# Kernel tuning notes

Measured on AMD Instinct MI355X. Metric: run time of the kernel, lower is better.

The kernel has to match this reference:

```python
import jax, jax.numpy as jnp
import numpy as np

PREFIX = 20000
LEAF = 50000
NONLEAF = 50000
NUMD = 8 * NONLEAF  # 400000 fine-depth nodes
C = 256


def setup_inputs() -> dict:
    key = jax.random.key(0)
    k1, k2 = jax.random.split(key)
    n_rows = PREFIX + LEAF + NUMD
    x = jax.random.normal(k1, (n_rows, C), dtype=jnp.float32)
    # xavier-uniform-like init for Downsample weights (C_out, C_in, 8)
    limit = float(np.sqrt(6.0 / (C + C * 8)))
    weights = jax.random.uniform(k2, (C, C, 8), dtype=jnp.float32,
                                 minval=-limit, maxval=limit)
    # children at depth-1: alternate leaf (-1) / non-leaf (+1) -> exactly LEAF leaves
    children = jnp.where(jnp.arange(LEAF + NONLEAF) % 2 == 0, -1, 1).astype(jnp.int32)
    return {"x": x, "weights": weights, "children": children,
            "numd": NUMD, "leaf_num": LEAF}


def reference(x, weights, children, numd, leaf_num):
    c = x.shape[1]
    # Downsample: groups of 8 fine nodes -> one coarse node.
    # torch: x.view(-1, 8*C) @ weights.flatten(1).t()
    outd = x[-numd:].reshape(-1, 8 * c) @ weights.reshape(c, 8 * c).T  # [numd/8, C]

    leaf_mask = children < 0                      # [nnum_prev]
    lm = leaf_mask.astype(jnp.int32)
    rank_leaf = jnp.cumsum(lm) - lm               # rank among leaf positions
    nlm = 1 - lm
    rank_nonleaf = jnp.cumsum(nlm) - nlm          # rank among non-leaf positions
    # out[leaf_mask] = x[-leaf_num-numd:-numd]; out[~leaf_mask] = outd
    idx = jnp.where(leaf_mask, rank_leaf, leaf_num + rank_nonleaf)
    x_leaf = x[-(leaf_num + numd):-numd]          # [leaf_num, C]
    combined = jnp.concatenate([x_leaf, outd], axis=0)
    merged = combined[idx]                        # [nnum_prev, C]

    prefix = x.shape[0] - leaf_num - numd
    return jnp.concatenate([x[:prefix], merged], axis=0)
```

## Files before the change

### kernel.cpp

```cpp
#include <hip/hip_runtime.h>
#include <hip/hip_bf16.h>

#define PREFIX_N 20000
#define LEAF_N   50000
#define CH_N     100000
#define CCOL     256
#define GK       2048
#define GM       50000
#define BM       64
#define BKF      128
#define NST      (GK / BKF)
#define TILES    ((GM + BM - 1) / BM)
#define NCOPYB   512
#define COPYROWS 70000

typedef float  f32x4v __attribute__((ext_vector_type(4)));
typedef __bf16 bf16x8 __attribute__((ext_vector_type(8)));
typedef short  s16x8  __attribute__((ext_vector_type(8)));

static __device__ __forceinline__ unsigned pk2(float a, float b) {
  __hip_bfloat16 ha = __float2bfloat16(a);
  __hip_bfloat16 hb = __float2bfloat16(b);
  unsigned short sa = __builtin_bit_cast(unsigned short, ha);
  unsigned short sb = __builtin_bit_cast(unsigned short, hb);
  return (unsigned)sa | ((unsigned)sb << 16);
}
static __device__ __forceinline__ uint4 pack8(const float4& x, const float4& y) {
  uint4 r;
  r.x = pk2(x.x, x.y); r.y = pk2(x.z, x.w);
  r.z = pk2(y.x, y.y); r.w = pk2(y.z, y.w);
  return r;
}

#define GLDS16(g, l) __builtin_amdgcn_global_load_lds(                      \
    (const __attribute__((address_space(1))) void*)(g),                     \
    (__attribute__((address_space(3))) void*)(l), 16, 0, 0)

__global__ __launch_bounds__(256) void prep_kernel(const float* __restrict__ W,
                                                   unsigned short* __restrict__ Wb,
                                                   const int* __restrict__ ch,
                                                   int* __restrict__ cnt) {
  if (blockIdx.x < 256) {
    int i = blockIdx.x * 256 + threadIdx.x;
    float4 a = ((const float4*)W)[i * 2];
    float4 b = ((const float4*)W)[i * 2 + 1];
    *(uint4*)&Wb[i * 8] = pack8(a, b);
  } else {
    int blk = blockIdx.x - 256;
    int gi = blk * 256 + threadIdx.x;
    int lm = (gi < CH_N && ch[gi] < 0) ? 1 : 0;
    unsigned long long mask = __ballot(lm);
    __shared__ int wsum[4];
    int lane = threadIdx.x & 63, w = threadIdx.x >> 6;
    if (lane == 0) wsum[w] = __popcll(mask);
    __syncthreads();
    if (threadIdx.x == 0) cnt[blk] = wsum[0] + wsum[1] + wsum[2] + wsum[3];
  }
}

__global__ __launch_bounds__(512) void scan_blocks(const int* __restrict__ cnt,
                                                   int* __restrict__ boff, int nb) {
  __shared__ int s[512];
  int t = threadIdx.x;
  int v = (t < nb) ? cnt[t] : 0;
  s[t] = v;
  __syncthreads();
  for (int d = 1; d < 512; d <<= 1) {
    int add = (t >= d) ? s[t - d] : 0;
    __syncthreads();
    s[t] += add;
    __syncthreads();
  }
  if (t < nb) boff[t] = s[t] - v;
}

__global__ __launch_bounds__(256) void rank_kernel(const int* __restrict__ ch,
                                                   const int* __restrict__ boff, int n,
                                                   int* __restrict__ rowof,
                                                   int* __restrict__ leafof) {
  int gi = blockIdx.x * 256 + threadIdx.x;
  int lane = threadIdx.x & 63, w = threadIdx.x >> 6;
  int lm = (gi < n && ch[gi] < 0) ? 1 : 0;
  unsigned long long mask = __ballot(lm);
  int lrank = __popcll(mask & ((1ull << lane) - 1ull));
  __shared__ int wcnt[4];
  if (lane == 63) wcnt[w] = lrank + lm;
  __syncthreads();
  int woff = 0;
  for (int i = 0; i < w; ++i) woff += wcnt[i];
  if (gi < n) {
    int rl = boff[blockIdx.x] + woff + lrank;
    if (lm) leafof[rl] = gi;
    else    rowof[gi - rl] = gi;
  }
}

__global__ __launch_bounds__(256, 2) void main_kernel(const float* __restrict__ x,
                                                      const float* __restrict__ A,
                                                      const unsigned short* __restrict__ Wb,
                                                      const int* __restrict__ rowof,
                                                      const int* __restrict__ leafof,
                                                      float* __restrict__ out) {
  __shared__ float Al[2][BM][BKF];
  __shared__ int tgt[BM];

  const int tid  = threadIdx.x;
  const int lane = tid & 63;
  const int w    = tid >> 6;

  if (blockIdx.x >= TILES) {
    int cb = blockIdx.x - TILES;
    for (int r0 = cb * 4; r0 < COPYROWS; r0 += NCOPYB * 4) {
      int j = r0 + w;
      if (j >= COPYROWS) break;
      const float* src;
      float* dst;
      if (j < PREFIX_N) {
        src = x + (size_t)j * CCOL;
        dst = out + (size_t)j * CCOL;
      } else {
        int r = j - PREFIX_N;
        src = x + (size_t)(PREFIX_N + r) * CCOL;
        dst = out + (size_t)(PREFIX_N + leafof[r]) * CCOL;
      }
      ((float4*)dst)[lane] = ((const float4*)src)[lane];
    }
    return;
  }

  const int tile = blockIdx.x;
  const int wn   = w;
  const int lr   = lane & 15, lq = lane >> 4;

  if (tid < BM) {
    int m = tile * BM + tid;
    tgt[tid] = (m < GM) ? (PREFIX_N + rowof[m]) : -1;
  }

  const float* asrc[8];
  int myrow = w * 16 + (lane >> 5);
#pragma unroll
  for (int i = 0; i < 8; ++i) {
    int r  = myrow + 2 * i;
    int gr = tile * BM + r;
    if (gr >= GM) gr = GM - 1;
    int chunk = (lane & 31) ^ (r & 7);
    asrc[i] = A + (size_t)gr * GK + chunk * 4;
  }

  const unsigned short* bb[4];
#pragma unroll
  for (int fn = 0; fn < 4; ++fn)
    bb[fn] = Wb + (size_t)(wn * 64 + fn * 16 + lr) * GK + lq * 8;

  f32x4v acc[4][4] = {};

#define ISSUE_A(kt_, buf_)                                                   \
  { _Pragma("unroll") for (int i = 0; i < 8; ++i)                            \
      GLDS16(asrc[i] + (kt_) * BKF, (char*)&Al[(buf_)][w * 16 + 2 * i][0]); }

  ISSUE_A(0, 0);
  ISSUE_A(1, 1);

#pragma unroll 1
  for (int kt = 0; kt < NST; ++kt) {
    if (kt < NST - 1) { asm volatile("s_waitcnt vmcnt(8)" ::: "memory"); }
    else              { asm volatile("s_waitcnt vmcnt(0)" ::: "memory"); }
    __builtin_amdgcn_s_barrier();

    const float* Ab = &Al[kt & 1][0][0];
#pragma unroll
    for (int ks = 0; ks < 4; ++ks) {
      s16x8 af[4], bf[4];
#pragma unroll
      for (int fm = 0; fm < 4; ++fm) {
        int row = fm * 16 + lr;
        int e   = ks * 8 + lq * 2;
        int p0  = ((e)     ^ (row & 7)) << 2;
        int p1  = ((e + 1) ^ (row & 7)) << 2;
        float4 u0 = *(const float4*)&Ab[row * BKF + p0];
        float4 u1 = *(const float4*)&Ab[row * BKF + p1];
        af[fm] = __builtin_bit_cast(s16x8, pack8(u0, u1));
      }
#pragma unroll
      for (int fn = 0; fn < 4; ++fn)
        bf[fn] = *(const s16x8*)&bb[fn][kt * BKF + ks * 32];
#pragma unroll
      for (int fm = 0; fm < 4; ++fm)
#pragma unroll
        for (int fn = 0; fn < 4; ++fn)
          acc[fm][fn] = __builtin_amdgcn_mfma_f32_16x16x32_bf16(
              __builtin_bit_cast(bf16x8, af[fm]),
              __builtin_bit_cast(bf16x8, bf[fn]),
              acc[fm][fn], 0, 0, 0);
    }

    asm volatile("s_waitcnt lgkmcnt(0)" ::: "memory");
    __builtin_amdgcn_s_barrier();
    if (kt + 2 < NST) ISSUE_A(kt + 2, kt & 1);
  }
#undef ISSUE_A

#pragma unroll
  for (int fm = 0; fm < 4; ++fm) {
    int mlb = fm * 16 + lq * 4;
    int t0 = tgt[mlb + 0], t1 = tgt[mlb + 1], t2 = tgt[mlb + 2], t3 = tgt[mlb + 3];
#pragma unroll
    for (int fn = 0; fn < 4; ++fn) {
      int col = wn * 64 + fn * 16 + lr;
      if (t0 >= 0) out[(size_t)t0 * CCOL + col] = acc[fm][fn][0];
      if (t1 >= 0) out[(size_t)t1 * CCOL + col] = acc[fm][fn][1];
      if (t2 >= 0) out[(size_t)t2 * CCOL + col] = acc[fm][fn][2];
      if (t3 >= 0) out[(size_t)t3 * CCOL + col] = acc[fm][fn][3];
    }
  }
}

extern "C" void kernel_launch(void* const* d_in, const int* in_sizes, int n_in,
                              void* d_out, int out_size, void* d_ws, size_t ws_size,
                              hipStream_t stream) {
  const float* x        = (const float*)d_in[0];
  const float* wts      = (const float*)d_in[1];
  const int*   children = (const int*)d_in[2];
  float*       out      = (float*)d_out;

  int* wsp    = (int*)d_ws;
  int* cnt    = wsp;
  int* boff   = wsp + 512;
  int* rowof  = wsp + 1024;
  int* leafof = wsp + 1024 + GM;
  unsigned short* Wb = (unsigned short*)((char*)d_ws + (1 << 20));

  const int nb = (CH_N + 255) / 256;

  prep_kernel<<<256 + nb, 256, 0, stream>>>(wts, Wb, children, cnt);
  scan_blocks<<<1, 512, 0, stream>>>(cnt, boff, nb);
  rank_kernel<<<nb, 256, 0, stream>>>(children, boff, CH_N, rowof, leafof);

  const float* A = x + (size_t)(PREFIX_N + LEAF_N) * CCOL;
  main_kernel<<<TILES + NCOPYB, 256, 0, stream>>>(x, A, Wb, rowof, leafof, out);
}
```

Measured before the change: 207.1 us.

## Stage A tile as bf16 in LDS via register prefetch, 512-thread blocks

```diff
diff --git a/kernel.cpp b/kernel.cpp
--- a/kernel.cpp
+++ b/kernel.cpp
@@ -31,10 +31,6 @@
   r.z = pk2(y.x, y.y); r.w = pk2(y.z, y.w);
   return r;
 }
-
-#define GLDS16(g, l) __builtin_amdgcn_global_load_lds(                      \
-    (const __attribute__((address_space(1))) void*)(g),                     \
-    (__attribute__((address_space(3))) void*)(l), 16, 0, 0)
 
 __global__ __launch_bounds__(256) void prep_kernel(const float* __restrict__ W,
                                                    unsigned short* __restrict__ Wb,
@@ -95,13 +91,13 @@
   }
 }
 
-__global__ __launch_bounds__(256, 2) void main_kernel(const float* __restrict__ x,
+__global__ __launch_bounds__(512, 4) void main_kernel(const float* __restrict__ x,
                                                       const float* __restrict__ A,
                                                       const unsigned short* __restrict__ Wb,
                                                       const int* __restrict__ rowof,
                                                       const int* __restrict__ leafof,
                                                       float* __restrict__ out) {
-  __shared__ float Al[2][BM][BKF];
+  __shared__ unsigned short Al[2][BM * BKF];
   __shared__ int tgt[BM];
 
   const int tid  = threadIdx.x;
@@ -110,7 +106,7 @@
 
   if (blockIdx.x >= TILES) {
     int cb = blockIdx.x - TILES;
-    for (int r0 = cb * 4; r0 < COPYROWS; r0 += NCOPYB * 4) {
+    for (int r0 = cb * 8; r0 < COPYROWS; r0 += NCOPYB * 8) {
       int j = r0 + w;
       if (j >= COPYROWS) break;
       const float* src;
@@ -129,7 +125,8 @@
   }
 
   const int tile = blockIdx.x;
-  const int wn   = w;
+  const int wm   = w >> 2;
+  const int wn   = w & 3;
   const int lr   = lane & 15, lq = lane >> 4;
 
   if (tid < BM) {
@@ -137,73 +134,82 @@
     tgt[tid] = (m < GM) ? (PREFIX_N + rowof[m]) : -1;
   }
 
-  const float* asrc[8];
-  int myrow = w * 16 + (lane >> 5);
-#pragma unroll
-  for (int i = 0; i < 8; ++i) {
-    int r  = myrow + 2 * i;
-    int gr = tile * BM + r;
-    if (gr >= GM) gr = GM - 1;
-    int chunk = (lane & 31) ^ (r & 7);
-    asrc[i] = A + (size_t)gr * GK + chunk * 4;
-  }
-
+  const int sr = tid >> 3;
+  const int sc = (tid & 7) * 16;
+  int agr = tile * BM + sr;
+  if (agr >= GM) agr = GM - 1;
+  const float* aptr = A + (size_t)agr * GK + sc;
+  const int g0  = (tid & 7) * 2;
+  const int pw0 = sr * BKF + ((g0)     ^ (sr & 15)) * 8;
+  const int pw1 = sr * BKF + ((g0 + 1) ^ (sr & 15)) * 8;
+
+  const int ar0 = (wm * 32 + lr) * BKF;
+  const int ar1 = ar0 + 16 * BKF;
   const unsigned short* bb[4];
 #pragma unroll
   for (int fn = 0; fn < 4; ++fn)
     bb[fn] = Wb + (size_t)(wn * 64 + fn * 16 + lr) * GK + lq * 8;
 
-  f32x4v acc[4][4] = {};
-
-#define ISSUE_A(kt_, buf_)                                                   \
-  { _Pragma("unroll") for (int i = 0; i < 8; ++i)                            \
-      GLDS16(asrc[i] + (kt_) * BKF, (char*)&Al[(buf_)][w * 16 + 2 * i][0]); }
-
-  ISSUE_A(0, 0);
-  ISSUE_A(1, 1);
+  f32x4v acc[2][4] = {};
+
+  float4 rP0, rP1, rP2, rP3, rQ0, rQ1, rQ2, rQ3;
+
+#define LOADA(d0, d1, d2, d3, kc)                                            \
+  { const float4* p_ = (const float4*)(aptr + (kc) * BKF);                   \
+    d0 = p_[0]; d1 = p_[1]; d2 = p_[2]; d3 = p_[3]; }
+
+#define STAGE(buf_, s0, s1, s2, s3)                                          \
+  { *(uint4*)&Al[(buf_)][pw0] = pack8(s0, s1);                               \
+    *(uint4*)&Al[(buf_)][pw1] = pack8(s2, s3); }
+
+#define COMPUTE(c_, kt_)                                                     \
+  { _Pragma("unroll") for (int ks = 0; ks < 4; ++ks) {                       \
+      int pg = ((ks * 4 + lq) ^ lr) * 8;                                     \
+      s16x8 af0 = *(const s16x8*)&Al[(c_)][ar0 + pg];                        \
+      s16x8 af1 = *(const s16x8*)&Al[(c_)][ar1 + pg];                        \
+      s16x8 bf[4];                                                           \
+      _Pragma("unroll") for (int fn = 0; fn < 4; ++fn)                       \
+        bf[fn] = *(const s16x8*)&bb[fn][(kt_) * BKF + ks * 32];              \
+      _Pragma("unroll") for (int fn = 0; fn < 4; ++fn) {                     \
+        acc[0][fn] = __builtin_amdgcn_mfma_f32_16x16x32_bf16(                \
+            __builtin_bit_cast(bf16x8, af0),                                 \
+            __builtin_bit_cast(bf16x8, bf[fn]), acc[0][fn], 0, 0, 0);        \
+        acc[1][fn] = __builtin_amdgcn_mfma_f32_16x16x32_bf16(                \
+            __builtin_bit_cast(bf16x8, af1),                                 \
+            __builtin_bit_cast(bf16x8, bf[fn]), acc[1][fn], 0, 0, 0);        \
+      } } }
+
+#define BARRIER()                                                            \
+  { asm volatile("s_waitcnt lgkmcnt(0)" ::: "memory");                       \
+    __builtin_amdgcn_s_barrier(); }
+
+#define BODY(kt_, c_, C0, C1, C2, C3, F0, F1, F2, F3)                        \
+  { if ((kt_) + 2 < NST) LOADA(F0, F1, F2, F3, (kt_) + 2);                   \
+    COMPUTE(c_, kt_);                                                        \
+    if ((kt_) + 1 < NST) {                                                   \
+      STAGE((c_) ^ 1, C0, C1, C2, C3);                                       \
+      BARRIER();                                                             \
+    } }
+
+  LOADA(rP0, rP1, rP2, rP3, 0);
+  LOADA(rQ0, rQ1, rQ2, rQ3, 1);
+  STAGE(0, rP0, rP1, rP2, rP3);
+  BARRIER();
 
 #pragma unroll 1
-  for (int kt = 0; kt < NST; ++kt) {
-    if (kt < NST - 1) { asm volatile("s_waitcnt vmcnt(8)" ::: "memory"); }
-    else              { asm volatile("s_waitcnt vmcnt(0)" ::: "memory"); }
-    __builtin_amdgcn_s_barrier();
-
-    const float* Ab = &Al[kt & 1][0][0];
+  for (int kt = 0; kt < NST; kt += 2) {
+    BODY(kt,     0, rQ0, rQ1, rQ2, rQ3, rP0, rP1, rP2, rP3);
+    BODY(kt + 1, 1, rP0, rP1, rP2, rP3, rQ0, rQ1, rQ2, rQ3);
+  }
+#undef BODY
+#undef BARRIER
+#undef COMPUTE
+#undef STAGE
+#undef LOADA
+
 #pragma unroll
-    for (int ks = 0; ks < 4; ++ks) {
-      s16x8 af[4], bf[4];
-#pragma unroll
-      for (int fm = 0; fm < 4; ++fm) {
-        int row = fm * 16 + lr;
-        int e   = ks * 8 + lq * 2;
-        int p0  = ((e)     ^ (row & 7)) << 2;
-        int p1  = ((e + 1) ^ (row & 7)) << 2;
-        float4 u0 = *(const float4*)&Ab[row * BKF + p0];
-        float4 u1 = *(const float4*)&Ab[row * BKF + p1];
-        af[fm] = __builtin_bit_cast(s16x8, pack8(u0, u1));
-      }
-#pragma unroll
-      for (int fn = 0; fn < 4; ++fn)
-        bf[fn] = *(const s16x8*)&bb[fn][kt * BKF + ks * 32];
-#pragma unroll
-      for (int fm = 0; fm < 4; ++fm)
-#pragma unroll
-        for (int fn = 0; fn < 4; ++fn)
-          acc[fm][fn] = __builtin_amdgcn_mfma_f32_16x16x32_bf16(
-              __builtin_bit_cast(bf16x8, af[fm]),
-              __builtin_bit_cast(bf16x8, bf[fn]),
-              acc[fm][fn], 0, 0, 0);
-    }
-
-    asm volatile("s_waitcnt lgkmcnt(0)" ::: "memory");
-    __builtin_amdgcn_s_barrier();
-    if (kt + 2 < NST) ISSUE_A(kt + 2, kt & 1);
-  }
-#undef ISSUE_A
-
-#pragma unroll
-  for (int fm = 0; fm < 4; ++fm) {
-    int mlb = fm * 16 + lq * 4;
+  for (int fm = 0; fm < 2; ++fm) {
+    int mlb = wm * 32 + fm * 16 + lq * 4;
     int t0 = tgt[mlb + 0], t1 = tgt[mlb + 1], t2 = tgt[mlb + 2], t3 = tgt[mlb + 3];
 #pragma unroll
     for (int fn = 0; fn < 4; ++fn) {
@@ -238,5 +244,5 @@
   rank_kernel<<<nb, 256, 0, stream>>>(children, boff, CH_N, rowof, leafof);
 
   const float* A = x + (size_t)(PREFIX_N + LEAF_N) * CCOL;
-  main_kernel<<<TILES + NCOPYB, 256, 0, stream>>>(x, A, Wb, rowof, leafof, out);
-}
+  main_kernel<<<TILES + NCOPYB, 512, 0, stream>>>(x, A, Wb, rowof, leafof, out);
+}
```

After: 326.3 us. 57.6% more time.

## Stage A tile as bf16 in LDS with halved row tile and two K halves

Applied to the files above, without the earlier changes.

```diff
diff --git a/kernel.cpp b/kernel.cpp
--- a/kernel.cpp
+++ b/kernel.cpp
@@ -7,9 +7,8 @@
 #define CCOL     256
 #define GK       2048
 #define GM       50000
-#define BM       64
-#define BKF      128
-#define NST      (GK / BKF)
+#define BM       32
+#define KH       1024
 #define TILES    ((GM + BM - 1) / BM)
 #define NCOPYB   512
 #define COPYROWS 70000
@@ -31,10 +30,6 @@
   r.z = pk2(y.x, y.y); r.w = pk2(y.z, y.w);
   return r;
 }
-
-#define GLDS16(g, l) __builtin_amdgcn_global_load_lds(                      \
-    (const __attribute__((address_space(1))) void*)(g),                     \
-    (__attribute__((address_space(3))) void*)(l), 16, 0, 0)
 
 __global__ __launch_bounds__(256) void prep_kernel(const float* __restrict__ W,
                                                    unsigned short* __restrict__ Wb,
@@ -101,7 +96,7 @@
                                                       const int* __restrict__ rowof,
                                                       const int* __restrict__ leafof,
                                                       float* __restrict__ out) {
-  __shared__ float Al[2][BM][BKF];
+  __shared__ unsigned short Al[BM][KH];
   __shared__ int tgt[BM];
 
   const int tid  = threadIdx.x;
@@ -110,8 +105,8 @@
 
   if (blockIdx.x >= TILES) {
     int cb = blockIdx.x - TILES;
-    for (int r0 = cb * 4; r0 < COPYROWS; r0 += NCOPYB * 4) {
-      int j = r0 + w;
+    for (int r0c = cb * 4; r0c < COPYROWS; r0c += NCOPYB * 4) {
+      int j = r0c + w;
       if (j >= COPYROWS) break;
       const float* src;
       float* dst;
@@ -137,56 +132,48 @@
     tgt[tid] = (m < GM) ? (PREFIX_N + rowof[m]) : -1;
   }
 
-  const float* asrc[8];
-  int myrow = w * 16 + (lane >> 5);
-#pragma unroll
-  for (int i = 0; i < 8; ++i) {
-    int r  = myrow + 2 * i;
-    int gr = tile * BM + r;
-    if (gr >= GM) gr = GM - 1;
-    int chunk = (lane & 31) ^ (r & 7);
-    asrc[i] = A + (size_t)gr * GK + chunk * 4;
-  }
+  const size_t r0 = (size_t)tile * BM;
+  const float* a0 = A + tid * 4;
 
   const unsigned short* bb[4];
 #pragma unroll
   for (int fn = 0; fn < 4; ++fn)
     bb[fn] = Wb + (size_t)(wn * 64 + fn * 16 + lr) * GK + lq * 8;
 
-  f32x4v acc[4][4] = {};
-
-#define ISSUE_A(kt_, buf_)                                                   \
-  { _Pragma("unroll") for (int i = 0; i < 8; ++i)                            \
-      GLDS16(asrc[i] + (kt_) * BKF, (char*)&Al[(buf_)][w * 16 + 2 * i][0]); }
-
-  ISSUE_A(0, 0);
-  ISSUE_A(1, 1);
+  f32x4v acc[2][4] = {};
+
+#define STAGE_BATCH(b2_, h_)                                                 \
+  { float4 v_[16];                                                           \
+    _Pragma("unroll") for (int i = 0; i < 16; ++i) {                         \
+      size_t gr = r0 + (b2_) * 16 + i;                                       \
+      if (gr >= GM) gr = GM - 1;                                             \
+      v_[i] = *(const float4*)(a0 + (gr << 11) + (h_) * KH);                 \
+    }                                                                        \
+    _Pragma("unroll") for (int i = 0; i < 16; ++i) {                         \
+      int r = (b2_) * 16 + i;                                                \
+      uint2 p_; p_.x = pk2(v_[i].x, v_[i].y); p_.y = pk2(v_[i].z, v_[i].w);  \
+      *(uint2*)((char*)&Al[r][0] +                                           \
+                ((((tid >> 1) ^ (r & 15)) << 4) + ((tid & 1) << 3))) = p_;   \
+    } }
 
 #pragma unroll 1
-  for (int kt = 0; kt < NST; ++kt) {
-    if (kt < NST - 1) { asm volatile("s_waitcnt vmcnt(8)" ::: "memory"); }
-    else              { asm volatile("s_waitcnt vmcnt(0)" ::: "memory"); }
-    __builtin_amdgcn_s_barrier();
-
-    const float* Ab = &Al[kt & 1][0][0];
-#pragma unroll
-    for (int ks = 0; ks < 4; ++ks) {
-      s16x8 af[4], bf[4];
-#pragma unroll
-      for (int fm = 0; fm < 4; ++fm) {
-        int row = fm * 16 + lr;
-        int e   = ks * 8 + lq * 2;
-        int p0  = ((e)     ^ (row & 7)) << 2;
-        int p1  = ((e + 1) ^ (row & 7)) << 2;
-        float4 u0 = *(const float4*)&Ab[row * BKF + p0];
-        float4 u1 = *(const float4*)&Ab[row * BKF + p1];
-        af[fm] = __builtin_bit_cast(s16x8, pack8(u0, u1));
-      }
+  for (int h = 0; h < 2; ++h) {
+    STAGE_BATCH(0, h);
+    STAGE_BATCH(1, h);
+    __syncthreads();
+
+#pragma unroll 8
+    for (int ks = 0; ks < KH / 32; ++ks) {
+      s16x8 af[2], bf[4];
+#pragma unroll
+      for (int fm = 0; fm < 2; ++fm)
+        af[fm] = *(const s16x8*)((const char*)&Al[fm * 16 + lr][0] +
+                                 ((((ks << 2) + lq) ^ lr) << 4));
 #pragma unroll
       for (int fn = 0; fn < 4; ++fn)
-        bf[fn] = *(const s16x8*)&bb[fn][kt * BKF + ks * 32];
-#pragma unroll
-      for (int fm = 0; fm < 4; ++fm)
+        bf[fn] = *(const s16x8*)&bb[fn][h * KH + ks * 32];
+#pragma unroll
+      for (int fm = 0; fm < 2; ++fm)
 #pragma unroll
         for (int fn = 0; fn < 4; ++fn)
           acc[fm][fn] = __builtin_amdgcn_mfma_f32_16x16x32_bf16(
@@ -194,15 +181,12 @@
               __builtin_bit_cast(bf16x8, bf[fn]),
               acc[fm][fn], 0, 0, 0);
     }
-
-    asm volatile("s_waitcnt lgkmcnt(0)" ::: "memory");
-    __builtin_amdgcn_s_barrier();
-    if (kt + 2 < NST) ISSUE_A(kt + 2, kt & 1);
-  }
-#undef ISSUE_A
-
-#pragma unroll
-  for (int fm = 0; fm < 4; ++fm) {
+    __syncthreads();
+  }
+#undef STAGE_BATCH
+
+#pragma unroll
+  for (int fm = 0; fm < 2; ++fm) {
     int mlb = fm * 16 + lq * 4;
     int t0 = tgt[mlb + 0], t1 = tgt[mlb + 1], t2 = tgt[mlb + 2], t3 = tgt[mlb + 3];
 #pragma unroll
```

Result: slower. 311.3 us (+50.3%).

## Pre-convert A to swizzled bf16 tiles in a separate streaming pass before GEMM

Applied to the files above, without the earlier changes.

```diff
diff --git a/kernel.cpp b/kernel.cpp
--- a/kernel.cpp
+++ b/kernel.cpp
@@ -8,11 +8,13 @@
 #define GK       2048
 #define GM       50000
 #define BM       64
-#define BKF      128
-#define NST      (GK / BKF)
+#define NKC      16
 #define TILES    ((GM + BM - 1) / BM)
-#define NCOPYB   512
-#define COPYROWS 70000
+#define GA       (GM * 256)
+#define GC       (70000 * 64)
+#define NBA      1512
+#define NBC      528
+#define NBW      8
 
 typedef float  f32x4v __attribute__((ext_vector_type(4)));
 typedef __bf16 bf16x8 __attribute__((ext_vector_type(8)));
@@ -36,26 +38,16 @@
     (const __attribute__((address_space(1))) void*)(g),                     \
     (__attribute__((address_space(3))) void*)(l), 16, 0, 0)
 
-__global__ __launch_bounds__(256) void prep_kernel(const float* __restrict__ W,
-                                                   unsigned short* __restrict__ Wb,
-                                                   const int* __restrict__ ch,
-                                                   int* __restrict__ cnt) {
-  if (blockIdx.x < 256) {
-    int i = blockIdx.x * 256 + threadIdx.x;
-    float4 a = ((const float4*)W)[i * 2];
-    float4 b = ((const float4*)W)[i * 2 + 1];
-    *(uint4*)&Wb[i * 8] = pack8(a, b);
-  } else {
-    int blk = blockIdx.x - 256;
-    int gi = blk * 256 + threadIdx.x;
-    int lm = (gi < CH_N && ch[gi] < 0) ? 1 : 0;
-    unsigned long long mask = __ballot(lm);
-    __shared__ int wsum[4];
-    int lane = threadIdx.x & 63, w = threadIdx.x >> 6;
-    if (lane == 0) wsum[w] = __popcll(mask);
-    __syncthreads();
-    if (threadIdx.x == 0) cnt[blk] = wsum[0] + wsum[1] + wsum[2] + wsum[3];
-  }
+__global__ __launch_bounds__(256) void count_leaves(const int* __restrict__ ch,
+                                                    int n, int* __restrict__ cnt) {
+  int gi = blockIdx.x * 256 + threadIdx.x;
+  int lm = (gi < n && ch[gi] < 0) ? 1 : 0;
+  unsigned long long mask = __ballot(lm);
+  __shared__ int wsum[4];
+  int lane = threadIdx.x & 63, w = threadIdx.x >> 6;
+  if (lane == 0) wsum[w] = __popcll(mask);
+  __syncthreads();
+  if (threadIdx.x == 0) cnt[blockIdx.x] = wsum[0] + wsum[1] + wsum[2] + wsum[3];
 }
 
 __global__ __launch_bounds__(512) void scan_blocks(const int* __restrict__ cnt,
@@ -95,96 +87,95 @@
   }
 }
 
-__global__ __launch_bounds__(256, 2) void main_kernel(const float* __restrict__ x,
-                                                      const float* __restrict__ A,
+__global__ __launch_bounds__(256) void stream_kernel(const float* __restrict__ x,
+                                                     const float* __restrict__ A,
+                                                     const float* __restrict__ W,
+                                                     unsigned short* __restrict__ Wb,
+                                                     uint4* __restrict__ Abg,
+                                                     const int* __restrict__ leafof,
+                                                     float* __restrict__ out) {
+  const int tid = threadIdx.x;
+  if (blockIdx.x < NBA) {
+    const int stride = NBA * 256;
+    for (int j = blockIdx.x * 256 + tid; j < GA; j += stride) {
+      const float4* ps = (const float4*)A + (size_t)j * 2;
+      float4 v0 = ps[0], v1 = ps[1];
+      int R = j >> 8, q = j & 255;
+      int kc = q >> 4, g = q & 15;
+      int gs = g ^ (R & 15);
+      size_t dgi = (((size_t)(R >> 6) * NKC + kc) * BM + (R & 63)) * 16 + gs;
+      Abg[dgi] = pack8(v0, v1);
+    }
+  } else if (blockIdx.x < NBA + NBC) {
+    const int stride = NBC * 256;
+    for (int c = (blockIdx.x - NBA) * 256 + tid; c < GC; c += stride) {
+      int row = c >> 6, col = c & 63;
+      int drow = (row < PREFIX_N) ? row : (PREFIX_N + leafof[row - PREFIX_N]);
+      ((float4*)out)[(size_t)drow * 64 + col] =
+          ((const float4*)x)[(size_t)row * 64 + col];
+    }
+  } else {
+    const int stride = NBW * 256;
+    for (int i = (blockIdx.x - NBA - NBC) * 256 + tid; i < 65536; i += stride) {
+      float4 a = ((const float4*)W)[i * 2];
+      float4 b = ((const float4*)W)[i * 2 + 1];
+      *(uint4*)&Wb[i * 8] = pack8(a, b);
+    }
+  }
+}
+
+__global__ __launch_bounds__(256, 3) void gemm_kernel(const uint4* __restrict__ Abg,
                                                       const unsigned short* __restrict__ Wb,
                                                       const int* __restrict__ rowof,
-                                                      const int* __restrict__ leafof,
                                                       float* __restrict__ out) {
-  __shared__ float Al[2][BM][BKF];
+  __shared__ char Al[2][16384];
   __shared__ int tgt[BM];
 
   const int tid  = threadIdx.x;
   const int lane = tid & 63;
   const int w    = tid >> 6;
-
-  if (blockIdx.x >= TILES) {
-    int cb = blockIdx.x - TILES;
-    for (int r0 = cb * 4; r0 < COPYROWS; r0 += NCOPYB * 4) {
-      int j = r0 + w;
-      if (j >= COPYROWS) break;
-      const float* src;
-      float* dst;
-      if (j < PREFIX_N) {
-        src = x + (size_t)j * CCOL;
-        dst = out + (size_t)j * CCOL;
-      } else {
-        int r = j - PREFIX_N;
-        src = x + (size_t)(PREFIX_N + r) * CCOL;
-        dst = out + (size_t)(PREFIX_N + leafof[r]) * CCOL;
-      }
-      ((float4*)dst)[lane] = ((const float4*)src)[lane];
-    }
-    return;
-  }
-
+  const int lr   = lane & 15, lq = lane >> 4;
   const int tile = blockIdx.x;
-  const int wn   = w;
-  const int lr   = lane & 15, lq = lane >> 4;
 
   if (tid < BM) {
     int m = tile * BM + tid;
     tgt[tid] = (m < GM) ? (PREFIX_N + rowof[m]) : -1;
   }
 
-  const float* asrc[8];
-  int myrow = w * 16 + (lane >> 5);
-#pragma unroll
-  for (int i = 0; i < 8; ++i) {
-    int r  = myrow + 2 * i;
-    int gr = tile * BM + r;
-    if (gr >= GM) gr = GM - 1;
-    int chunk = (lane & 31) ^ (r & 7);
-    asrc[i] = A + (size_t)gr * GK + chunk * 4;
-  }
+  const char* src0 = (const char*)(Abg + (size_t)tile * (NKC * BM * 16))
+                     + w * 4096 + lane * 16;
 
   const unsigned short* bb[4];
 #pragma unroll
   for (int fn = 0; fn < 4; ++fn)
-    bb[fn] = Wb + (size_t)(wn * 64 + fn * 16 + lr) * GK + lq * 8;
+    bb[fn] = Wb + (size_t)(w * 64 + fn * 16 + lr) * GK + lq * 8;
 
   f32x4v acc[4][4] = {};
 
-#define ISSUE_A(kt_, buf_)                                                   \
-  { _Pragma("unroll") for (int i = 0; i < 8; ++i)                            \
-      GLDS16(asrc[i] + (kt_) * BKF, (char*)&Al[(buf_)][w * 16 + 2 * i][0]); }
-
-  ISSUE_A(0, 0);
-  ISSUE_A(1, 1);
+#define ISSUE(kc_, buf_)                                                     \
+  { _Pragma("unroll") for (int i = 0; i < 4; ++i)                            \
+      GLDS16(src0 + (kc_) * 16384 + i * 1024, &Al[(buf_)][(w * 4 + i) * 1024]); }
+
+  ISSUE(0, 0);
+  ISSUE(1, 1);
 
 #pragma unroll 1
-  for (int kt = 0; kt < NST; ++kt) {
-    if (kt < NST - 1) { asm volatile("s_waitcnt vmcnt(8)" ::: "memory"); }
+  for (int kc = 0; kc < NKC; ++kc) {
+    if (kc < NKC - 1) { asm volatile("s_waitcnt vmcnt(4)" ::: "memory"); }
     else              { asm volatile("s_waitcnt vmcnt(0)" ::: "memory"); }
     __builtin_amdgcn_s_barrier();
 
-    const float* Ab = &Al[kt & 1][0][0];
+    const char* Ab = Al[kc & 1];
 #pragma unroll
     for (int ks = 0; ks < 4; ++ks) {
       s16x8 af[4], bf[4];
 #pragma unroll
-      for (int fm = 0; fm < 4; ++fm) {
-        int row = fm * 16 + lr;
-        int e   = ks * 8 + lq * 2;
-        int p0  = ((e)     ^ (row & 7)) << 2;
-        int p1  = ((e + 1) ^ (row & 7)) << 2;
-        float4 u0 = *(const float4*)&Ab[row * BKF + p0];
-        float4 u1 = *(const float4*)&Ab[row * BKF + p1];
-        af[fm] = __builtin_bit_cast(s16x8, pack8(u0, u1));
-      }
+      for (int fm = 0; fm < 4; ++fm)
+        af[fm] = *(const s16x8*)(Ab + (fm * 16 + lr) * 256 +
+                                 (((ks * 4 + lq) ^ lr) << 4));
 #pragma unroll
       for (int fn = 0; fn < 4; ++fn)
-        bf[fn] = *(const s16x8*)&bb[fn][kt * BKF + ks * 32];
+        bf[fn] = *(const s16x8*)&bb[fn][kc * 128 + ks * 32];
 #pragma unroll
       for (int fm = 0; fm < 4; ++fm)
 #pragma unroll
@@ -197,9 +188,9 @@
 
     asm volatile("s_waitcnt lgkmcnt(0)" ::: "memory");
     __builtin_amdgcn_s_barrier();
-    if (kt + 2 < NST) ISSUE_A(kt + 2, kt & 1);
-  }
-#undef ISSUE_A
+    if (kc + 2 < NKC) ISSUE(kc + 2, kc & 1);
+  }
+#undef ISSUE
 
 #pragma unroll
   for (int fm = 0; fm < 4; ++fm) {
@@ -207,7 +198,7 @@
     int t0 = tgt[mlb + 0], t1 = tgt[mlb + 1], t2 = tgt[mlb + 2], t3 = tgt[mlb + 3];
 #pragma unroll
     for (int fn = 0; fn < 4; ++fn) {
-      int col = wn * 64 + fn * 16 + lr;
+      int col = w * 64 + fn * 16 + lr;
       if (t0 >= 0) out[(size_t)t0 * CCOL + col] = acc[fm][fn][0];
       if (t1 >= 0) out[(size_t)t1 * CCOL + col] = acc[fm][fn][1];
       if (t2 >= 0) out[(size_t)t2 * CCOL + col] = acc[fm][fn][2];
@@ -230,13 +221,16 @@
   int* rowof  = wsp + 1024;
   int* leafof = wsp + 1024 + GM;
   unsigned short* Wb = (unsigned short*)((char*)d_ws + (1 << 20));
+  uint4* Abg = (uint4*)((char*)d_ws + (2u << 20));
 
   const int nb = (CH_N + 255) / 256;
 
-  prep_kernel<<<256 + nb, 256, 0, stream>>>(wts, Wb, children, cnt);
+  count_leaves<<<nb, 256, 0, stream>>>(children, CH_N, cnt);
   scan_blocks<<<1, 512, 0, stream>>>(cnt, boff, nb);
   rank_kernel<<<nb, 256, 0, stream>>>(children, boff, CH_N, rowof, leafof);
 
   const float* A = x + (size_t)(PREFIX_N + LEAF_N) * CCOL;
-  main_kernel<<<TILES + NCOPYB, 256, 0, stream>>>(x, A, Wb, rowof, leafof, out);
-}
+  stream_kernel<<<NBA + NBC + NBW, 256, 0, stream>>>(x, A, wts, Wb, Abg,
+                                                     leafof, out);
+  gemm_kernel<<<TILES, 256, 0, stream>>>(Abg, Wb, rowof, out);
+}
```

After: 320.2 us. +54.6%, slower.
